# Kernel tuning notes

Hardware: AMD Instinct MI355X
Metric: run time of the kernel (lower is better)

Reference implementation:

```python
import jax, jax.numpy as jnp
import numpy as np

N_HEADS = 8  # from init_kwargs; only used for the softmax scale


def setup_inputs() -> dict:
    key = jax.random.key(0)
    k1, k2, k3 = jax.random.split(key, 3)
    B, S, D = 4, 4096, 1024
    inputs = jax.random.normal(k1, (B, S, 2 * D), dtype=jnp.float32)
    W_qkv = jax.random.normal(k2, (2 * D, 3 * D), dtype=jnp.float32) * (1.0 / np.sqrt(2 * D))
    W_ff = jax.random.normal(k3, (D, D), dtype=jnp.float32) * (1.0 / np.sqrt(D))
    b_ff = jnp.zeros((D,), dtype=jnp.float32)
    return {"inputs": inputs, "W_qkv": W_qkv, "W_ff": W_ff, "b_ff": b_ff}


def reference(inputs, W_qkv, W_ff, b_ff):
    D = W_ff.shape[0]
    dim_head = D / N_HEADS
    scale = 1.0 / np.sqrt(dim_head)
    kqv = inputs @ W_qkv                       # [B, S, 3D]
    k, q, v = jnp.split(kqv, 3, axis=-1)        # chunk order in source: k, q, v
    scores = jnp.einsum('bqd,bkd->bqk', q, k) * scale   # [B, S, S]
    attn = jax.nn.softmax(scores, axis=-1)
    # dropout_p is undefined in the buggy source; treated as eval-mode identity
    out = jnp.einsum('bqk,bkd->bqd', attn, v)   # [B, S, D]
    return out @ W_ff + b_ff
```

## Files before the change

kernel.cpp:

```cpp
#include <hip/hip_runtime.h>

typedef unsigned short u16;
using bf16x8 = __attribute__((ext_vector_type(8))) __bf16;
using f32x4  = __attribute__((ext_vector_type(4))) float;
using u16x8  = __attribute__((ext_vector_type(8))) u16;

__device__ __forceinline__ u16 f2bf(float f) {
    unsigned u = __builtin_bit_cast(unsigned, f);
    u += 0x7FFFu + ((u >> 16) & 1u);
    return (u16)(u >> 16);
}
__device__ __forceinline__ float bf2f(u16 h) {
    unsigned u = ((unsigned)h) << 16;
    return __builtin_bit_cast(float, u);
}
__device__ __forceinline__ u16 to_bf(float f) { return f2bf(f); }
__device__ __forceinline__ u16 to_bf(u16 h)   { return h; }

__device__ __forceinline__ void gload_lds16(const u16* g, u16* l) {
    __builtin_amdgcn_global_load_lds(
        (const __attribute__((address_space(1))) unsigned int*)g,
        (__attribute__((address_space(3))) unsigned int*)l,
        16, 0, 0);
}

__global__ __launch_bounds__(256) void k_cvt_f32_bf16(const float* __restrict__ in,
                                                      u16* __restrict__ out, long n) {
    long i = ((long)blockIdx.x * 256 + threadIdx.x) * 8;
    if (i + 8 > n) return;
    f32x4 a = *(const f32x4*)(in + i);
    f32x4 b = *(const f32x4*)(in + i + 4);
    u16x8 o;
    o[0] = f2bf(a[0]); o[1] = f2bf(a[1]); o[2] = f2bf(a[2]); o[3] = f2bf(a[3]);
    o[4] = f2bf(b[0]); o[5] = f2bf(b[1]); o[6] = f2bf(b[2]); o[7] = f2bf(b[3]);
    *(u16x8*)(out + i) = o;
}

template <typename T>
__global__ __launch_bounds__(256) void k_transpose_bf16(
    const T* __restrict__ in, long in_rs, long in_bs,
    u16* __restrict__ out, long out_rs, long out_bs, int R, int C) {
    __shared__ u16 tile[32][33];
    const int b = blockIdx.z;
    const T* ip = in + (long)b * in_bs;
    u16* op = out + (long)b * out_bs;
    const int tx = threadIdx.x, ty = threadIdx.y;
    const long r0 = (long)blockIdx.y * 32, c0 = (long)blockIdx.x * 32;
#pragma unroll
    for (int i = 0; i < 4; ++i) {
        int r = ty + i * 8;
        tile[r][tx] = to_bf(ip[(r0 + r) * in_rs + c0 + tx]);
    }
    __syncthreads();
#pragma unroll
    for (int i = 0; i < 4; ++i) {
        int c = ty + i * 8;
        op[(c0 + c) * out_rs + r0 + tx] = tile[tx][c];
    }
}

__global__ __launch_bounds__(256) void k_rowsum_recip(const u16* __restrict__ P,
                                                      float* __restrict__ out, int C) {
    const long row = blockIdx.x;
    const u16* p = P + row * (long)C;
    float s = 0.f;
    for (int c = threadIdx.x * 8; c < C; c += 256 * 8) {
        u16x8 v = *(const u16x8*)(p + c);
#pragma unroll
        for (int j = 0; j < 8; ++j) s += bf2f(v[j]);
    }
#pragma unroll
    for (int off = 32; off > 0; off >>= 1) s += __shfl_down(s, off);
    __shared__ float wsum[4];
    const int lane = threadIdx.x & 63, wid = threadIdx.x >> 6;
    if (lane == 0) wsum[wid] = s;
    __syncthreads();
    if (threadIdx.x == 0) out[row] = 1.0f / (wsum[0] + wsum[1] + wsum[2] + wsum[3]);
}


#define LGK(n) asm volatile("s_waitcnt lgkmcnt(" #n ")" ::: "memory")
#define VMC(n) asm volatile("s_waitcnt vmcnt(" #n ")" ::: "memory")
#define SCHB   __builtin_amdgcn_sched_barrier(0)
#define BAR    __builtin_amdgcn_s_barrier()
#define PRIO1  __builtin_amdgcn_s_setprio(1)
#define PRIO0  __builtin_amdgcn_s_setprio(0)
#define SWZ(b) ((b) ^ ((((b) >> 9) & 1) << 5))

template <int EPI>
__global__ __launch_bounds__(512, 4) void k_gemm3b(
    const u16* __restrict__ Ag, long lda, long sA,
    const u16* __restrict__ Bg, long ldb, long sB,
    void* __restrict__ Cv, long ldc, long sC,
    int K, float scale, const float* __restrict__ rrowZ, long sR,
    const float* __restrict__ bias) {
    __shared__ __align__(16) u16 As[3][128 * 32];
    __shared__ __align__(16) u16 Bs[3][256 * 32];

    const int tid = threadIdx.x;
    const int lane = tid & 63, wid = tid >> 6;
    const int wm = wid >> 2, wn = wid & 3;
    const int z = blockIdx.z;
    const long m0 = (long)blockIdx.y * 128;
    const long n0 = (long)blockIdx.x * 256;
    const u16* A = Ag + (long)z * sA;
    const u16* B = Bg + (long)z * sB;

    long aSrc, bSrc0, bSrc1;
    {
        int dg = SWZ(tid * 16);
        aSrc = (m0 + (dg >> 6)) * lda + ((dg & 63) >> 1);
        dg = SWZ(tid * 16);
        bSrc0 = (n0 + (dg >> 6)) * ldb + ((dg & 63) >> 1);
        dg = SWZ(8192 + tid * 16);
        bSrc1 = (n0 + (dg >> 6)) * ldb + ((dg & 63) >> 1);
    }
    const int r16 = lane & 15, g = lane >> 4;
    const int vA = SWZ((wm * 64 + r16) * 64 + g * 16);
    const int vB = SWZ((wn * 64 + r16) * 64 + g * 16);

#define STG(bb, kt) do { \
        gload_lds16(A + aSrc + (kt), &As[bb][wid * 512]); \
        gload_lds16(B + bSrc0 + (kt), &Bs[bb][wid * 512]); \
        gload_lds16(B + bSrc1 + (kt), &Bs[bb][4096 + wid * 512]); } while (0)
#define LD4_A(bb) do { _Pragma("unroll") for (int _i = 0; _i < 4; ++_i) \
        afr[_i] = *(const bf16x8*)((const char*)&As[bb][0] + vA + _i * 1024); } while (0)
#define LD4_B(bb) do { _Pragma("unroll") for (int _i = 0; _i < 4; ++_i) \
        bfr[_i] = *(const bf16x8*)((const char*)&Bs[bb][0] + vB + _i * 1024); } while (0)
#define MM16() do { \
        _Pragma("unroll") for (int mf = 0; mf < 4; ++mf) \
        _Pragma("unroll") for (int nf = 0; nf < 4; ++nf) \
            acc[mf][nf] = __builtin_amdgcn_mfma_f32_16x16x32_bf16( \
                afr[mf], bfr[nf], acc[mf][nf], 0, 0, 0); } while (0)

    f32x4 acc[4][4] = {};
    bf16x8 afr[4], bfr[4];

    const int NT = K >> 5;
    STG(0, 0); STG(1, 32);
    VMC(3); SCHB;
    BAR; SCHB;

    int b0 = 0, b1 = 1, b2 = 2;
    for (int t = 0; t < NT; ++t) {
        LD4_A(b0); LD4_B(b0);
        if (t + 2 < NT) STG(b2, (long)(t + 2) * 32);
        LGK(0); SCHB;
        PRIO1; MM16(); PRIO0;
        if (t + 2 < NT) { VMC(3); }
        else if (t + 1 < NT) { VMC(0); }
        SCHB; BAR; SCHB;
        int tm = b0; b0 = b1; b1 = b2; b2 = tm;
    }

    const int r_in = (lane >> 4) * 4;
    const int c_in = lane & 15;
    const float* rr = (EPI == 2) ? (rrowZ + (long)z * sR) : nullptr;
#pragma unroll
    for (int mf = 0; mf < 4; ++mf) {
#pragma unroll
        for (int nf = 0; nf < 4; ++nf) {
            const long cg = n0 + wn * 64 + nf * 16 + c_in;
#pragma unroll
            for (int j = 0; j < 4; ++j) {
                const long rg = m0 + wm * 64 + mf * 16 + r_in + j;
                float v = acc[mf][nf][j];
                if constexpr (EPI == 0) {
                    ((u16*)Cv)[(long)z * sC + rg * ldc + cg] = f2bf(v);
                } else if constexpr (EPI == 1) {
                    ((u16*)Cv)[(long)z * sC + rg * ldc + cg] = f2bf(__expf(v * scale));
                } else if constexpr (EPI == 2) {
                    ((u16*)Cv)[(long)z * sC + rg * ldc + cg] = f2bf(v * rr[rg]);
                } else {
                    ((float*)Cv)[(long)z * sC + rg * ldc + cg] = v + bias[cg];
                }
            }
        }
    }
#undef MM16
#undef LD4_A
#undef LD4_B
#undef STG
}

extern "C" void kernel_launch(void* const* d_in, const int* in_sizes, int n_in,
                              void* d_out, int out_size, void* d_ws, size_t ws_size,
                              hipStream_t stream) {
    (void)in_sizes; (void)n_in; (void)out_size;
    const int S = 4096;
    const long BS = 4L * S;
    const float* x_f    = (const float*)d_in[0];
    const float* Wqkv_f = (const float*)d_in[1];
    const float* Wff_f  = (const float*)d_in[2];
    const float* bff    = (const float*)d_in[3];
    float* out = (float*)d_out;

    const size_t need4 = 67108864UL + 12582912UL + 2097152UL + 100663296UL +
                         33554432UL + 4UL * 33554432UL + 33554432UL + 65536UL;
    const bool batched = ws_size >= need4;
    const int Z = batched ? 4 : 1;

    char* p = (char*)d_ws;
    u16* x_bf  = (u16*)p; p += BS * 2048 * 2;
    u16* WqkvT = (u16*)p; p += 3072L * 2048 * 2;
    u16* WffT  = (u16*)p; p += 1024L * 1024 * 2;
    u16* kqv   = (u16*)p; p += BS * 3072 * 2;
    u16* vT    = (u16*)p; p += 4L * 1024 * 4096 * 2;
    u16* probs = (u16*)p; p += (long)Z * 4096L * 4096 * 2;
    u16* attn  = (u16*)p; p += BS * 1024 * 2;
    float* rrow = (float*)p; p += (long)Z * 4096L * 4;

    k_cvt_f32_bf16<<<dim3((unsigned)(BS * 2048 / 2048)), 256, 0, stream>>>(x_f, x_bf, BS * 2048);
    k_transpose_bf16<float><<<dim3(3072 / 32, 2048 / 32, 1), dim3(32, 8), 0, stream>>>(
        Wqkv_f, 3072, 0, WqkvT, 2048, 0, 2048, 3072);
    k_transpose_bf16<float><<<dim3(1024 / 32, 1024 / 32, 1), dim3(32, 8), 0, stream>>>(
        Wff_f, 1024, 0, WffT, 1024, 0, 1024, 1024);

    k_gemm3b<0><<<dim3(3072 / 256, 16384 / 128, 1), 512, 0, stream>>>(
        x_bf, 2048, 0, WqkvT, 2048, 0, kqv, 3072, 0, 2048, 0.f, nullptr, 0, nullptr);

    k_transpose_bf16<u16><<<dim3(1024 / 32, 4096 / 32, 4), dim3(32, 8), 0, stream>>>(
        kqv + 2048, 3072, (long)S * 3072, vT, 4096, 1024L * 4096, 4096, 1024);

    const float scale = 0.08838834764831845f;
    for (int b = 0; b < 4; b += Z) {
        const u16* kbase = kqv + (long)b * S * 3072;
        k_gemm3b<1><<<dim3(4096 / 256, 4096 / 128, Z), 512, 0, stream>>>(
            kbase + 1024, 3072, (long)S * 3072, kbase, 3072, (long)S * 3072,
            probs, 4096, (long)S * S, 1024, scale, nullptr, 0, nullptr);
        k_rowsum_recip<<<Z * 4096, 256, 0, stream>>>(probs, rrow, 4096);
        k_gemm3b<2><<<dim3(1024 / 256, 4096 / 128, Z), 512, 0, stream>>>(
            probs, 4096, (long)S * S, vT + (long)b * 1024 * 4096, 4096, 1024L * 4096,
            attn + (long)b * S * 1024, 1024, (long)S * 1024,
            4096, 0.f, rrow, 4096, nullptr);
    }

    k_gemm3b<3><<<dim3(1024 / 256, 16384 / 128, 1), 512, 0, stream>>>(
        attn, 1024, 0, WffT, 1024, 0, out, 1024, 0, 1024, 0.f, nullptr, 0, bff);
}
```

Before: 619.1 us.

## Fuse softmax row-sum into exp GEMM epilogue and drop explicit LDS wait

The exp-score GEMM epilogue now accumulates per-row partial sums of the fp32 exponentials. It reduces them across lanes and waves through LDS and writes one partial per column block. A tiny kernel then sums the 16 partials per row and takes the reciprocal. This replaces the separate pass that re-read the whole bf16 probability matrix. The main loop also drops the explicit lgkmcnt(0) wait and one sched barrier, leaving LDS-read waits to the compiler; this may change how MFMA issue overlaps with LDS reads. Sums now come from unrounded fp32 values rather than the stored bf16 values.

```diff
diff --git a/kernel.cpp b/kernel.cpp
--- a/kernel.cpp
+++ b/kernel.cpp
@@ -59,27 +59,19 @@
     }
 }
 
-__global__ __launch_bounds__(256) void k_rowsum_recip(const u16* __restrict__ P,
-                                                      float* __restrict__ out, int C) {
-    const long row = blockIdx.x;
-    const u16* p = P + row * (long)C;
+__global__ __launch_bounds__(256) void k_psum_recip(const float* __restrict__ psum,
+                                                    float* __restrict__ rrow,
+                                                    int nx, long total) {
+    long idx = (long)blockIdx.x * 256 + threadIdx.x;
+    if (idx >= total) return;
+    const long z = idx >> 12, row = idx & 4095;
+    const float* p = psum + (z * nx) * 4096 + row;
     float s = 0.f;
-    for (int c = threadIdx.x * 8; c < C; c += 256 * 8) {
-        u16x8 v = *(const u16x8*)(p + c);
-#pragma unroll
-        for (int j = 0; j < 8; ++j) s += bf2f(v[j]);
-    }
-#pragma unroll
-    for (int off = 32; off > 0; off >>= 1) s += __shfl_down(s, off);
-    __shared__ float wsum[4];
-    const int lane = threadIdx.x & 63, wid = threadIdx.x >> 6;
-    if (lane == 0) wsum[wid] = s;
-    __syncthreads();
-    if (threadIdx.x == 0) out[row] = 1.0f / (wsum[0] + wsum[1] + wsum[2] + wsum[3]);
-}
-
-
-#define LGK(n) asm volatile("s_waitcnt lgkmcnt(" #n ")" ::: "memory")
+    for (int x = 0; x < nx; ++x) s += p[(long)x * 4096];
+    rrow[idx] = 1.0f / s;
+}
+
+
 #define VMC(n) asm volatile("s_waitcnt vmcnt(" #n ")" ::: "memory")
 #define SCHB   __builtin_amdgcn_sched_barrier(0)
 #define BAR    __builtin_amdgcn_s_barrier()
@@ -93,7 +85,7 @@
     const u16* __restrict__ Bg, long ldb, long sB,
     void* __restrict__ Cv, long ldc, long sC,
     int K, float scale, const float* __restrict__ rrowZ, long sR,
-    const float* __restrict__ bias) {
+    const float* __restrict__ bias, float* __restrict__ psum) {
     __shared__ __align__(16) u16 As[3][128 * 32];
     __shared__ __align__(16) u16 Bs[3][256 * 32];
 
@@ -110,7 +102,6 @@
     {
         int dg = SWZ(tid * 16);
         aSrc = (m0 + (dg >> 6)) * lda + ((dg & 63) >> 1);
-        dg = SWZ(tid * 16);
         bSrc0 = (n0 + (dg >> 6)) * ldb + ((dg & 63) >> 1);
         dg = SWZ(8192 + tid * 16);
         bSrc1 = (n0 + (dg >> 6)) * ldb + ((dg & 63) >> 1);
@@ -145,17 +136,23 @@
     for (int t = 0; t < NT; ++t) {
         LD4_A(b0); LD4_B(b0);
         if (t + 2 < NT) STG(b2, (long)(t + 2) * 32);
-        LGK(0); SCHB;
         PRIO1; MM16(); PRIO0;
         if (t + 2 < NT) { VMC(3); }
         else if (t + 1 < NT) { VMC(0); }
-        SCHB; BAR; SCHB;
+        BAR; SCHB;
         int tm = b0; b0 = b1; b1 = b2; b2 = tm;
     }
 
     const int r_in = (lane >> 4) * 4;
     const int c_in = lane & 15;
     const float* rr = (EPI == 2) ? (rrowZ + (long)z * sR) : nullptr;
+    float rsum[4][4];
+    if constexpr (EPI == 1) {
+#pragma unroll
+        for (int a = 0; a < 4; ++a)
+#pragma unroll
+            for (int b = 0; b < 4; ++b) rsum[a][b] = 0.f;
+    }
 #pragma unroll
     for (int mf = 0; mf < 4; ++mf) {
 #pragma unroll
@@ -168,13 +165,35 @@
                 if constexpr (EPI == 0) {
                     ((u16*)Cv)[(long)z * sC + rg * ldc + cg] = f2bf(v);
                 } else if constexpr (EPI == 1) {
-                    ((u16*)Cv)[(long)z * sC + rg * ldc + cg] = f2bf(__expf(v * scale));
+                    float e = __expf(v * scale);
+                    ((u16*)Cv)[(long)z * sC + rg * ldc + cg] = f2bf(e);
+                    rsum[mf][j] += e;
                 } else if constexpr (EPI == 2) {
                     ((u16*)Cv)[(long)z * sC + rg * ldc + cg] = f2bf(v * rr[rg]);
                 } else {
                     ((float*)Cv)[(long)z * sC + rg * ldc + cg] = v + bias[cg];
                 }
             }
+        }
+    }
+    if constexpr (EPI == 1) {
+        float* ps = (float*)&As[0][0];
+#pragma unroll
+        for (int mf = 0; mf < 4; ++mf) {
+#pragma unroll
+            for (int j = 0; j < 4; ++j) {
+                float s = rsum[mf][j];
+#pragma unroll
+                for (int w = 1; w < 16; w <<= 1) s += __shfl_xor(s, w);
+                if ((lane & 15) == 0)
+                    ps[(wm * 64 + mf * 16 + (lane >> 4) * 4 + j) * 4 + wn] = s;
+            }
+        }
+        __syncthreads();
+        if (tid < 128) {
+            float s = ps[tid * 4] + ps[tid * 4 + 1] + ps[tid * 4 + 2] + ps[tid * 4 + 3];
+            const long M = (long)gridDim.y * 128;
+            psum[((long)z * gridDim.x + blockIdx.x) * M + m0 + tid] = s;
         }
     }
 #undef MM16
@@ -196,7 +215,8 @@
     float* out = (float*)d_out;
 
     const size_t need4 = 67108864UL + 12582912UL + 2097152UL + 100663296UL +
-                         33554432UL + 4UL * 33554432UL + 33554432UL + 65536UL;
+                         33554432UL + 4UL * 33554432UL + 33554432UL + 65536UL +
+                         4UL * 16 * 4096 * 4;
     const bool batched = ws_size >= need4;
     const int Z = batched ? 4 : 1;
 
@@ -209,6 +229,7 @@
     u16* probs = (u16*)p; p += (long)Z * 4096L * 4096 * 2;
     u16* attn  = (u16*)p; p += BS * 1024 * 2;
     float* rrow = (float*)p; p += (long)Z * 4096L * 4;
+    float* psum = (float*)p; p += (long)Z * 16 * 4096 * 4;
 
     k_cvt_f32_bf16<<<dim3((unsigned)(BS * 2048 / 2048)), 256, 0, stream>>>(x_f, x_bf, BS * 2048);
     k_transpose_bf16<float><<<dim3(3072 / 32, 2048 / 32, 1), dim3(32, 8), 0, stream>>>(
@@ -217,7 +238,7 @@
         Wff_f, 1024, 0, WffT, 1024, 0, 1024, 1024);
 
     k_gemm3b<0><<<dim3(3072 / 256, 16384 / 128, 1), 512, 0, stream>>>(
-        x_bf, 2048, 0, WqkvT, 2048, 0, kqv, 3072, 0, 2048, 0.f, nullptr, 0, nullptr);
+        x_bf, 2048, 0, WqkvT, 2048, 0, kqv, 3072, 0, 2048, 0.f, nullptr, 0, nullptr, nullptr);
 
     k_transpose_bf16<u16><<<dim3(1024 / 32, 4096 / 32, 4), dim3(32, 8), 0, stream>>>(
         kqv + 2048, 3072, (long)S * 3072, vT, 4096, 1024L * 4096, 4096, 1024);
@@ -227,14 +248,15 @@
         const u16* kbase = kqv + (long)b * S * 3072;
         k_gemm3b<1><<<dim3(4096 / 256, 4096 / 128, Z), 512, 0, stream>>>(
             kbase + 1024, 3072, (long)S * 3072, kbase, 3072, (long)S * 3072,
-            probs, 4096, (long)S * S, 1024, scale, nullptr, 0, nullptr);
-        k_rowsum_recip<<<Z * 4096, 256, 0, stream>>>(probs, rrow, 4096);
+            probs, 4096, (long)S * S, 1024, scale, nullptr, 0, nullptr, psum);
+        k_psum_recip<<<(Z * 4096 + 255) / 256, 256, 0, stream>>>(
+            psum, rrow, 16, (long)Z * 4096);
         k_gemm3b<2><<<dim3(1024 / 256, 4096 / 128, Z), 512, 0, stream>>>(
             probs, 4096, (long)S * S, vT + (long)b * 1024 * 4096, 4096, 1024L * 4096,
             attn + (long)b * S * 1024, 1024, (long)S * 1024,
-            4096, 0.f, rrow, 4096, nullptr);
+            4096, 0.f, rrow, 4096, nullptr, nullptr);
     }
 
     k_gemm3b<3><<<dim3(1024 / 256, 16384 / 128, 1), 512, 0, stream>>>(
-        attn, 1024, 0, WffT, 1024, 0, out, 1024, 0, 1024, 0.f, nullptr, 0, bff);
-}
+        attn, 1024, 0, WffT, 1024, 0, out, 1024, 0, 1024, 0.f, nullptr, 0, bff, nullptr);
+}
```

Result: no change. 618.4 us (-0.1%).
